# Kernel tuning notes

Measured on AMD Instinct MI355X. Metric: run time of the kernel, lower is better.

## Reference

```python
import jax, jax.numpy as jnp
import numpy as np

N, DIN, DOUT, E, K = 65536, 256, 256, 8, 2

def setup_inputs() -> dict:
    key = jax.random.key(0)
    k1, k2, k3, k4 = jax.random.split(key, 4)
    x = jax.random.normal(k1, (N, DIN), dtype=jnp.float32)
    Wr = jax.random.normal(k2, (DIN, E), dtype=jnp.float32) * (DIN ** -0.5)   # router Linear (no bias)
    We = jax.random.normal(k3, (E, DIN, DOUT), dtype=jnp.float32) * (DIN ** -0.5)  # expert Linear weights
    be = jax.random.normal(k4, (E, DOUT), dtype=jnp.float32) * 0.01               # expert Linear biases
    return {"x": x, "Wr": Wr, "We": We, "be": be}

def reference(x, Wr, We, be):
    # router: softmax over experts (eval mode -> no noise)
    probs = jax.nn.softmax(x @ Wr, axis=1)                    # [N, E]
    w, sel = jax.lax.top_k(probs, K)                          # [N, K]
    w = w / jnp.sum(w, axis=1, keepdims=True)                 # renormalize top-k weights
    # dense combine weights: scatter top-k weights back to [N, E]
    combine = jnp.zeros_like(probs).at[jnp.arange(x.shape[0])[:, None], sel].add(w)
    # all-expert outputs, then weighted combine (same math as gather/matmul/index_add loop)
    y_all = jnp.einsum('ni,eio->neo', x, We) + be[None, :, :]  # [N, E, DOUT]
    out = jnp.einsum('neo,ne->no', y_all, combine)             # [N, DOUT]
    return out
```

## Files before the change

kernel.cpp:

```cpp
#include <hip/hip_runtime.h>

#define N_TOK 65536
#define DIN   256
#define DOUT  256
#define NEXP  8
#define NPAIR 28

typedef __bf16 bf16x8 __attribute__((ext_vector_type(8)));
typedef __bf16 bf16x4 __attribute__((ext_vector_type(4)));
typedef float  f32x4  __attribute__((ext_vector_type(4)));

__device__ __forceinline__ void cp16_g2l(const void* g, void* l) {
  auto gp = (const __attribute__((address_space(1))) unsigned int*)(unsigned long long)g;
  auto lp = (__attribute__((address_space(3))) unsigned int*)(unsigned long long)l;
  __builtin_amdgcn_global_load_lds(gp, lp, 16, 0, 0);
}

__global__ __launch_bounds__(256) void prep_kernel(const float* __restrict__ We,
                                                   __bf16* __restrict__ Wt,
                                                   int* __restrict__ cnt) {
  __shared__ float T[64 * 65];
  int bid = blockIdx.x;
  if (bid == 0 && threadIdx.x < NPAIR) cnt[threadIdx.x] = 0;
  int e = bid >> 4;
  int tk = (bid >> 2) & 3, tn = bid & 3;
  int k0 = tk * 64, n0 = tn * 64;
  int tid = threadIdx.x;
  int cr = tid >> 6;
  int cc = tid & 63;
#pragma unroll
  for (int i = 0; i < 16; i++) {
    int k = i * 4 + cr;
    T[cc * 65 + k] = We[(size_t)(e * 256 + k0 + k) * 256 + n0 + cc];
  }
  __syncthreads();
#pragma unroll
  for (int i = 0; i < 16; i++) {
    int n = i * 4 + cr;
    Wt[(size_t)(e * 256 + n0 + n) * 256 + k0 + cc] = (__bf16)T[n * 65 + cc];
  }
}

__global__ __launch_bounds__(256) void router_kernel(const float* __restrict__ x,
                                                     const float* __restrict__ Wr,
                                                     __bf16* __restrict__ xb,
                                                     int* __restrict__ cnt,
                                                     unsigned short* __restrict__ pidx,
                                                     float* __restrict__ pw) {
  __shared__ float WrL[DIN * NEXP];
  __shared__ int lcnt[NPAIR];
  __shared__ int gbase[NPAIR];
  int tid = threadIdx.x;
  for (int j = tid; j < DIN * NEXP / 4; j += 256)
    *(float4*)&WrL[j * 4] = *(const float4*)&Wr[j * 4];
  if (tid < NPAIR) lcnt[tid] = 0;
  __syncthreads();

  int token = blockIdx.x * 256 + tid;
  const float4* xr = (const float4*)(x + (size_t)token * DIN);
  __bf16* xbr = xb + (size_t)token * DIN;

  float acc[NEXP];
#pragma unroll
  for (int e = 0; e < NEXP; e++) acc[e] = 0.f;

#pragma unroll 8
  for (int i4 = 0; i4 < DIN / 4; i4++) {
    float4 v = xr[i4];
    bf16x4 bv;
    bv[0] = (__bf16)v.x; bv[1] = (__bf16)v.y; bv[2] = (__bf16)v.z; bv[3] = (__bf16)v.w;
    *(bf16x4*)(xbr + i4 * 4) = bv;
    const float* w0 = &WrL[(i4 * 4) * NEXP];
#pragma unroll
    for (int e = 0; e < NEXP; e++)
      acc[e] += v.x * w0[e] + v.y * w0[NEXP + e] + v.z * w0[2 * NEXP + e] + v.w * w0[3 * NEXP + e];
  }

  int best = 0;
#pragma unroll
  for (int e = 1; e < NEXP; e++) if (acc[e] > acc[best]) best = e;
  int sec = (best == 0) ? 1 : 0;
#pragma unroll
  for (int e = 0; e < NEXP; e++)
    if (e != best && e != sec && acc[e] > acc[sec]) sec = e;
  float l3 = -1e30f;
#pragma unroll
  for (int e = 0; e < NEXP; e++)
    if (e != best && e != sec) l3 = fmaxf(l3, acc[e]);

  float diff = acc[sec] - acc[best];
  bool need = (acc[sec] - l3) < 5e-3f;
  if (__any(need)) {
    if (need) {
      double d[NEXP];
#pragma unroll
      for (int e = 0; e < NEXP; e++) d[e] = 0.0;
      for (int i4 = 0; i4 < DIN / 4; i4++) {
        float4 v = xr[i4];
        const float* w0 = &WrL[(i4 * 4) * NEXP];
#pragma unroll
        for (int e = 0; e < NEXP; e++)
          d[e] += (double)v.x * w0[e] + (double)v.y * w0[NEXP + e] +
                  (double)v.z * w0[2 * NEXP + e] + (double)v.w * w0[3 * NEXP + e];
      }
      best = 0;
#pragma unroll
      for (int e = 1; e < NEXP; e++) if (d[e] > d[best]) best = e;
      sec = (best == 0) ? 1 : 0;
#pragma unroll
      for (int e = 0; e < NEXP; e++)
        if (e != best && e != sec && d[e] > d[sec]) sec = e;
      diff = (float)(d[sec] - d[best]);
    }
  }

  float wb = 1.f / (1.f + expf(diff));
  int a, b2; float wa;
  if (best < sec) { a = best; b2 = sec; wa = wb; }
  else            { a = sec;  b2 = best; wa = 1.f - wb; }
  int p = a * (15 - a) / 2 + (b2 - a - 1);

  int lpos = atomicAdd(&lcnt[p], 1);
  __syncthreads();
  if (tid < NPAIR) gbase[tid] = atomicAdd(&cnt[tid], lcnt[tid]);
  __syncthreads();
  int pos = gbase[p] + lpos;
  pidx[p * N_TOK + pos] = (unsigned short)token;
  pw[p * N_TOK + pos] = wa;
}

__global__ __launch_bounds__(256) void moe_gemm_kernel(const __bf16* __restrict__ xb,
                                                       const __bf16* __restrict__ Wt,
                                                       const float* __restrict__ be,
                                                       const int* __restrict__ cnt,
                                                       const unsigned short* __restrict__ pidx,
                                                       const float* __restrict__ pw,
                                                       float* __restrict__ out) {
  __shared__ __bf16 As[128 * 64];
  __shared__ unsigned short tokL[128];
  __shared__ float wL[128];
  __shared__ int meta[4];

  int tid = threadIdx.x;
  int tile = blockIdx.x >> 2;
  int nh = blockIdx.x & 3;

  if (tid == 0) {
    int s = 0, pp = -1, lt = 0, c = 0;
    for (int q = 0; q < NPAIR; q++) {
      int cq = cnt[q];
      int tq = (cq + 127) >> 7;
      if (tile < s + tq) { pp = q; lt = tile - s; c = cq; break; }
      s += tq;
    }
    meta[0] = pp; meta[1] = lt; meta[2] = c;
  }
  __syncthreads();
  int p = meta[0];
  if (p < 0) return;
  int lt = meta[1], cnt_p = meta[2];

  int a = 0, rem = p;
  while (rem >= 7 - a) { rem -= 7 - a; a++; }
  int b2 = a + 1 + rem;
  int r0 = lt * 128;

  if (tid < 128) {
    int gr = r0 + tid;
    tokL[tid] = (gr < cnt_p) ? pidx[p * N_TOK + gr] : (unsigned short)0;
    wL[tid]   = (gr < cnt_p) ? pw[p * N_TOK + gr] : 0.f;
  }
  __syncthreads();

  const int lane = tid & 63, wid = tid >> 6;
  const int wm = wid & 1, wn = wid >> 1;
  const int c16 = lane & 15, quad = lane >> 4;

  const int r_base = tid >> 3;
  const int s8 = (tid & 7) ^ (r_base & 7);
  size_t grow[4];
#pragma unroll
  for (int i = 0; i < 4; i++)
    grow[i] = (size_t)tokL[r_base + 32 * i] * DIN + s8 * 8;

  const __bf16* WtA = Wt + ((size_t)a * DOUT + nh * 64) * DIN;
  const __bf16* WtB = Wt + ((size_t)b2 * DOUT + nh * 64) * DIN;

  f32x4 accA[4][2], accB[4][2];
#pragma unroll
  for (int mi = 0; mi < 4; mi++)
#pragma unroll
    for (int ni = 0; ni < 2; ni++)
#pragma unroll
      for (int r = 0; r < 4; r++) { accA[mi][ni][r] = 0.f; accB[mi][ni][r] = 0.f; }

  for (int kc = 0; kc < 4; kc++) {
#pragma unroll
    for (int i = 0; i < 4; i++) {
      int slot = tid + 256 * i;
      cp16_g2l(xb + grow[i] + kc * 64, &As[slot * 8]);
    }
    __builtin_amdgcn_s_waitcnt(0x0F70);
    __syncthreads();
#pragma unroll
    for (int ks = 0; ks < 2; ks++) {
      bf16x8 af[4], ba[2], bb[2];
#pragma unroll
      for (int mi = 0; mi < 4; mi++) {
        int row = wm * 64 + mi * 16 + c16;
        int oct = ks * 4 + quad;
        af[mi] = *(const bf16x8*)&As[(row * 8 + (oct ^ (row & 7))) * 8];
      }
#pragma unroll
      for (int ni = 0; ni < 2; ni++) {
        int col = wn * 32 + ni * 16 + c16;
        int koff = kc * 64 + ks * 32 + quad * 8;
        ba[ni] = *(const bf16x8*)&WtA[(size_t)col * DIN + koff];
        bb[ni] = *(const bf16x8*)&WtB[(size_t)col * DIN + koff];
      }
#pragma unroll
      for (int mi = 0; mi < 4; mi++)
#pragma unroll
        for (int ni = 0; ni < 2; ni++) {
          accA[mi][ni] = __builtin_amdgcn_mfma_f32_16x16x32_bf16(af[mi], ba[ni], accA[mi][ni], 0, 0, 0);
          accB[mi][ni] = __builtin_amdgcn_mfma_f32_16x16x32_bf16(af[mi], bb[ni], accB[mi][ni], 0, 0, 0);
        }
    }
    __syncthreads();
  }

#pragma unroll
  for (int ni = 0; ni < 2; ni++) {
    int gcol = nh * 64 + wn * 32 + ni * 16 + c16;
    float bea = be[a * DOUT + gcol];
    float beb = be[b2 * DOUT + gcol];
#pragma unroll
    for (int mi = 0; mi < 4; mi++) {
#pragma unroll
      for (int r = 0; r < 4; r++) {
        int row = wm * 64 + mi * 16 + quad * 4 + r;
        if (r0 + row < cnt_p) {
          float w = wL[row];
          out[(size_t)tokL[row] * DOUT + gcol] =
              w * (accA[mi][ni][r] + bea) + (1.f - w) * (accB[mi][ni][r] + beb);
        }
      }
    }
  }
}

extern "C" void kernel_launch(void* const* d_in, const int* in_sizes, int n_in,
                              void* d_out, int out_size, void* d_ws, size_t ws_size,
                              hipStream_t stream) {
  const float* x  = (const float*)d_in[0];
  const float* Wr = (const float*)d_in[1];
  const float* We = (const float*)d_in[2];
  const float* be = (const float*)d_in[3];
  float* out = (float*)d_out;

  char* w = (char*)d_ws;
  __bf16* Wt = (__bf16*)w;
  __bf16* xb = (__bf16*)(w + (1u << 20));
  int* cnt = (int*)(w + (33u << 20));
  unsigned short* pidx = (unsigned short*)(w + (33u << 20) + 512);
  float* pw = (float*)(w + (33u << 20) + 512 + (size_t)NPAIR * N_TOK * 2);

  prep_kernel<<<128, 256, 0, stream>>>(We, Wt, cnt);
  router_kernel<<<N_TOK / 256, 256, 0, stream>>>(x, Wr, xb, cnt, pidx, pw);
  moe_gemm_kernel<<<540 * 4, 256, 0, stream>>>(xb, Wt, be, cnt, pidx, pw, out);
}
```

Before: 224.1 us.

## Split router across four lanes per token and stage full A tile once in GEMM

The prep kernel now uses smaller 32x32 transpose tiles across more blocks. The router assigns four threads per token with a transposed router weight layout and reduces the partial dot products with shuffles, which gives more parallelism and coalesced loads. The grouped GEMM loads the whole 128x256 activation tile into LDS once per block and loops over all four output quarters, so the gathered rows are no longer fetched four times. The cost is 64KB of LDS per block, which limits occupancy to about two blocks per CU, and fewer GEMM blocks overall.

```diff
diff --git a/kernel.cpp b/kernel.cpp
--- a/kernel.cpp
+++ b/kernel.cpp
@@ -19,25 +19,25 @@
 __global__ __launch_bounds__(256) void prep_kernel(const float* __restrict__ We,
                                                    __bf16* __restrict__ Wt,
                                                    int* __restrict__ cnt) {
-  __shared__ float T[64 * 65];
+  __shared__ float T[32 * 33];
   int bid = blockIdx.x;
   if (bid == 0 && threadIdx.x < NPAIR) cnt[threadIdx.x] = 0;
-  int e = bid >> 4;
-  int tk = (bid >> 2) & 3, tn = bid & 3;
-  int k0 = tk * 64, n0 = tn * 64;
+  int e = bid >> 6;
+  int t = bid & 63;
+  int k0 = (t >> 3) * 32, n0 = (t & 7) * 32;
   int tid = threadIdx.x;
-  int cr = tid >> 6;
-  int cc = tid & 63;
-#pragma unroll
-  for (int i = 0; i < 16; i++) {
-    int k = i * 4 + cr;
-    T[cc * 65 + k] = We[(size_t)(e * 256 + k0 + k) * 256 + n0 + cc];
-  }
-  __syncthreads();
-#pragma unroll
-  for (int i = 0; i < 16; i++) {
-    int n = i * 4 + cr;
-    Wt[(size_t)(e * 256 + n0 + n) * 256 + k0 + cc] = (__bf16)T[n * 65 + cc];
+  int cc = tid & 31;
+  int rr = tid >> 5;
+#pragma unroll
+  for (int i = 0; i < 4; i++) {
+    int k = i * 8 + rr;
+    T[cc * 33 + k] = We[(size_t)(e * 256 + k0 + k) * 256 + n0 + cc];
+  }
+  __syncthreads();
+#pragma unroll
+  for (int i = 0; i < 4; i++) {
+    int n = i * 8 + rr;
+    Wt[(size_t)(e * 256 + n0 + n) * 256 + k0 + cc] = (__bf16)T[n * 33 + cc];
   }
 }
 
@@ -47,61 +47,74 @@
                                                      int* __restrict__ cnt,
                                                      unsigned short* __restrict__ pidx,
                                                      float* __restrict__ pw) {
-  __shared__ float WrL[DIN * NEXP];
+  __shared__ float WrT[NEXP * DIN];
   __shared__ int lcnt[NPAIR];
   __shared__ int gbase[NPAIR];
   int tid = threadIdx.x;
-  for (int j = tid; j < DIN * NEXP / 4; j += 256)
-    *(float4*)&WrL[j * 4] = *(const float4*)&Wr[j * 4];
+  for (int i = tid; i < NEXP * DIN; i += 256) {
+    int e = i >> 8, d = i & 255;
+    WrT[i] = Wr[d * NEXP + e];
+  }
   if (tid < NPAIR) lcnt[tid] = 0;
   __syncthreads();
 
-  int token = blockIdx.x * 256 + tid;
-  const float4* xr = (const float4*)(x + (size_t)token * DIN);
-  __bf16* xbr = xb + (size_t)token * DIN;
+  int token = blockIdx.x * 64 + (tid >> 2);
+  int q = tid & 3;
+  const float* xrow = x + (size_t)token * DIN;
+  const float4* xr4 = (const float4*)xrow;
+  __bf16* xbrow = xb + (size_t)token * DIN;
 
   float acc[NEXP];
 #pragma unroll
   for (int e = 0; e < NEXP; e++) acc[e] = 0.f;
 
-#pragma unroll 8
-  for (int i4 = 0; i4 < DIN / 4; i4++) {
-    float4 v = xr[i4];
+#pragma unroll 4
+  for (int j = 0; j < 16; j++) {
+    int c = j * 4 + q;
+    float4 v = xr4[c];
     bf16x4 bv;
     bv[0] = (__bf16)v.x; bv[1] = (__bf16)v.y; bv[2] = (__bf16)v.z; bv[3] = (__bf16)v.w;
-    *(bf16x4*)(xbr + i4 * 4) = bv;
-    const float* w0 = &WrL[(i4 * 4) * NEXP];
+    *(bf16x4*)(xbrow + c * 4) = bv;
+#pragma unroll
+    for (int e = 0; e < NEXP; e++) {
+      float4 w = *(const float4*)&WrT[e * DIN + c * 4];
+      acc[e] += v.x * w.x + v.y * w.y + v.z * w.z + v.w * w.w;
+    }
+  }
+#pragma unroll
+  for (int e = 0; e < NEXP; e++) {
+    acc[e] += __shfl_xor(acc[e], 1);
+    acc[e] += __shfl_xor(acc[e], 2);
+  }
+
+  int p = -1, lpos = 0, a = 0, b2 = 0;
+  float wa = 0.f;
+  if (q == 0) {
+    int best = 0;
+#pragma unroll
+    for (int e = 1; e < NEXP; e++) if (acc[e] > acc[best]) best = e;
+    int sec = (best == 0) ? 1 : 0;
 #pragma unroll
     for (int e = 0; e < NEXP; e++)
-      acc[e] += v.x * w0[e] + v.y * w0[NEXP + e] + v.z * w0[2 * NEXP + e] + v.w * w0[3 * NEXP + e];
-  }
-
-  int best = 0;
-#pragma unroll
-  for (int e = 1; e < NEXP; e++) if (acc[e] > acc[best]) best = e;
-  int sec = (best == 0) ? 1 : 0;
-#pragma unroll
-  for (int e = 0; e < NEXP; e++)
-    if (e != best && e != sec && acc[e] > acc[sec]) sec = e;
-  float l3 = -1e30f;
-#pragma unroll
-  for (int e = 0; e < NEXP; e++)
-    if (e != best && e != sec) l3 = fmaxf(l3, acc[e]);
-
-  float diff = acc[sec] - acc[best];
-  bool need = (acc[sec] - l3) < 5e-3f;
-  if (__any(need)) {
-    if (need) {
+      if (e != best && e != sec && acc[e] > acc[sec]) sec = e;
+    float l3 = -1e30f;
+#pragma unroll
+    for (int e = 0; e < NEXP; e++)
+      if (e != best && e != sec) l3 = fmaxf(l3, acc[e]);
+
+    float diff = acc[sec] - acc[best];
+    if (acc[sec] - l3 < 5e-3f) {
       double d[NEXP];
 #pragma unroll
       for (int e = 0; e < NEXP; e++) d[e] = 0.0;
-      for (int i4 = 0; i4 < DIN / 4; i4++) {
-        float4 v = xr[i4];
-        const float* w0 = &WrL[(i4 * 4) * NEXP];
-#pragma unroll
-        for (int e = 0; e < NEXP; e++)
-          d[e] += (double)v.x * w0[e] + (double)v.y * w0[NEXP + e] +
-                  (double)v.z * w0[2 * NEXP + e] + (double)v.w * w0[3 * NEXP + e];
+      for (int c = 0; c < 64; c++) {
+        float4 v = xr4[c];
+#pragma unroll
+        for (int e = 0; e < NEXP; e++) {
+          const float* w = &WrT[e * DIN + c * 4];
+          d[e] += (double)v.x * w[0] + (double)v.y * w[1] +
+                  (double)v.z * w[2] + (double)v.w * w[3];
+        }
       }
       best = 0;
 #pragma unroll
@@ -112,45 +125,47 @@
         if (e != best && e != sec && d[e] > d[sec]) sec = e;
       diff = (float)(d[sec] - d[best]);
     }
-  }
-
-  float wb = 1.f / (1.f + expf(diff));
-  int a, b2; float wa;
-  if (best < sec) { a = best; b2 = sec; wa = wb; }
-  else            { a = sec;  b2 = best; wa = 1.f - wb; }
-  int p = a * (15 - a) / 2 + (b2 - a - 1);
-
-  int lpos = atomicAdd(&lcnt[p], 1);
+
+    float wb = 1.f / (1.f + expf(diff));
+    if (best < sec) { a = best; b2 = sec; wa = wb; }
+    else            { a = sec;  b2 = best; wa = 1.f - wb; }
+    p = a * (15 - a) / 2 + (b2 - a - 1);
+    lpos = atomicAdd(&lcnt[p], 1);
+  }
   __syncthreads();
   if (tid < NPAIR) gbase[tid] = atomicAdd(&cnt[tid], lcnt[tid]);
   __syncthreads();
-  int pos = gbase[p] + lpos;
-  pidx[p * N_TOK + pos] = (unsigned short)token;
-  pw[p * N_TOK + pos] = wa;
-}
-
-__global__ __launch_bounds__(256) void moe_gemm_kernel(const __bf16* __restrict__ xb,
-                                                       const __bf16* __restrict__ Wt,
-                                                       const float* __restrict__ be,
-                                                       const int* __restrict__ cnt,
-                                                       const unsigned short* __restrict__ pidx,
-                                                       const float* __restrict__ pw,
-                                                       float* __restrict__ out) {
-  __shared__ __bf16 As[128 * 64];
+  if (q == 0) {
+    int pos = gbase[p] + lpos;
+    pidx[p * N_TOK + pos] = (unsigned short)token;
+    pw[p * N_TOK + pos] = wa;
+  }
+}
+
+__global__ __launch_bounds__(256, 2) void moe_gemm_kernel(const __bf16* __restrict__ xb,
+                                                          const __bf16* __restrict__ Wt,
+                                                          const float* __restrict__ be,
+                                                          const int* __restrict__ cnt,
+                                                          const unsigned short* __restrict__ pidx,
+                                                          const float* __restrict__ pw,
+                                                          float* __restrict__ out) {
+  __shared__ __bf16 As[128 * 256];
   __shared__ unsigned short tokL[128];
   __shared__ float wL[128];
-  __shared__ int meta[4];
+  __shared__ int cntL[NPAIR];
+  __shared__ int meta[3];
 
   int tid = threadIdx.x;
-  int tile = blockIdx.x >> 2;
-  int nh = blockIdx.x & 3;
-
+  int tile = blockIdx.x;
+
+  if (tid < NPAIR) cntL[tid] = cnt[tid];
+  __syncthreads();
   if (tid == 0) {
     int s = 0, pp = -1, lt = 0, c = 0;
-    for (int q = 0; q < NPAIR; q++) {
-      int cq = cnt[q];
+    for (int qq = 0; qq < NPAIR; qq++) {
+      int cq = cntL[qq];
       int tq = (cq + 127) >> 7;
-      if (tile < s + tq) { pp = q; lt = tile - s; c = cq; break; }
+      if (tile < s + tq) { pp = qq; lt = tile - s; c = cq; break; }
       s += tq;
     }
     meta[0] = pp; meta[1] = lt; meta[2] = c;
@@ -172,49 +187,45 @@
   }
   __syncthreads();
 
+#pragma unroll
+  for (int i = 0; i < 16; i++) {
+    int g = tid + 256 * i;
+    int r = g >> 5, sl = g & 31;
+    int s = sl ^ (r & 7);
+    cp16_g2l(xb + (size_t)tokL[r] * DIN + s * 8, &As[g * 8]);
+  }
+  __builtin_amdgcn_s_waitcnt(0x0F70);
+  __syncthreads();
+
   const int lane = tid & 63, wid = tid >> 6;
   const int wm = wid & 1, wn = wid >> 1;
   const int c16 = lane & 15, quad = lane >> 4;
 
-  const int r_base = tid >> 3;
-  const int s8 = (tid & 7) ^ (r_base & 7);
-  size_t grow[4];
-#pragma unroll
-  for (int i = 0; i < 4; i++)
-    grow[i] = (size_t)tokL[r_base + 32 * i] * DIN + s8 * 8;
-
-  const __bf16* WtA = Wt + ((size_t)a * DOUT + nh * 64) * DIN;
-  const __bf16* WtB = Wt + ((size_t)b2 * DOUT + nh * 64) * DIN;
-
-  f32x4 accA[4][2], accB[4][2];
-#pragma unroll
-  for (int mi = 0; mi < 4; mi++)
-#pragma unroll
-    for (int ni = 0; ni < 2; ni++)
-#pragma unroll
-      for (int r = 0; r < 4; r++) { accA[mi][ni][r] = 0.f; accB[mi][ni][r] = 0.f; }
-
-  for (int kc = 0; kc < 4; kc++) {
-#pragma unroll
-    for (int i = 0; i < 4; i++) {
-      int slot = tid + 256 * i;
-      cp16_g2l(xb + grow[i] + kc * 64, &As[slot * 8]);
-    }
-    __builtin_amdgcn_s_waitcnt(0x0F70);
-    __syncthreads();
-#pragma unroll
-    for (int ks = 0; ks < 2; ks++) {
+  const __bf16* WtA = Wt + (size_t)a  * DOUT * DIN;
+  const __bf16* WtB = Wt + (size_t)b2 * DOUT * DIN;
+
+  for (int nh = 0; nh < 4; nh++) {
+    f32x4 accA[4][2], accB[4][2];
+#pragma unroll
+    for (int mi = 0; mi < 4; mi++)
+#pragma unroll
+      for (int ni = 0; ni < 2; ni++)
+#pragma unroll
+        for (int r = 0; r < 4; r++) { accA[mi][ni][r] = 0.f; accB[mi][ni][r] = 0.f; }
+
+#pragma unroll
+    for (int kstep = 0; kstep < 8; kstep++) {
       bf16x8 af[4], ba[2], bb[2];
+      int o = kstep * 4 + quad;
 #pragma unroll
       for (int mi = 0; mi < 4; mi++) {
         int row = wm * 64 + mi * 16 + c16;
-        int oct = ks * 4 + quad;
-        af[mi] = *(const bf16x8*)&As[(row * 8 + (oct ^ (row & 7))) * 8];
-      }
+        af[mi] = *(const bf16x8*)&As[row * 256 + (o ^ (row & 7)) * 8];
+      }
+      int koff = kstep * 32 + quad * 8;
 #pragma unroll
       for (int ni = 0; ni < 2; ni++) {
-        int col = wn * 32 + ni * 16 + c16;
-        int koff = kc * 64 + ks * 32 + quad * 8;
+        int col = nh * 64 + wn * 32 + ni * 16 + c16;
         ba[ni] = *(const bf16x8*)&WtA[(size_t)col * DIN + koff];
         bb[ni] = *(const bf16x8*)&WtB[(size_t)col * DIN + koff];
       }
@@ -226,23 +237,22 @@
           accB[mi][ni] = __builtin_amdgcn_mfma_f32_16x16x32_bf16(af[mi], bb[ni], accB[mi][ni], 0, 0, 0);
         }
     }
-    __syncthreads();
-  }
-
-#pragma unroll
-  for (int ni = 0; ni < 2; ni++) {
-    int gcol = nh * 64 + wn * 32 + ni * 16 + c16;
-    float bea = be[a * DOUT + gcol];
-    float beb = be[b2 * DOUT + gcol];
-#pragma unroll
-    for (int mi = 0; mi < 4; mi++) {
-#pragma unroll
-      for (int r = 0; r < 4; r++) {
-        int row = wm * 64 + mi * 16 + quad * 4 + r;
-        if (r0 + row < cnt_p) {
-          float w = wL[row];
-          out[(size_t)tokL[row] * DOUT + gcol] =
-              w * (accA[mi][ni][r] + bea) + (1.f - w) * (accB[mi][ni][r] + beb);
+
+#pragma unroll
+    for (int ni = 0; ni < 2; ni++) {
+      int gcol = nh * 64 + wn * 32 + ni * 16 + c16;
+      float bea = be[a * DOUT + gcol];
+      float beb = be[b2 * DOUT + gcol];
+#pragma unroll
+      for (int mi = 0; mi < 4; mi++) {
+#pragma unroll
+        for (int r = 0; r < 4; r++) {
+          int row = wm * 64 + mi * 16 + quad * 4 + r;
+          if (r0 + row < cnt_p) {
+            float w = wL[row];
+            out[(size_t)tokL[row] * DOUT + gcol] =
+                w * (accA[mi][ni][r] + bea) + (1.f - w) * (accB[mi][ni][r] + beb);
+          }
         }
       }
     }
@@ -265,7 +275,7 @@
   unsigned short* pidx = (unsigned short*)(w + (33u << 20) + 512);
   float* pw = (float*)(w + (33u << 20) + 512 + (size_t)NPAIR * N_TOK * 2);
 
-  prep_kernel<<<128, 256, 0, stream>>>(We, Wt, cnt);
-  router_kernel<<<N_TOK / 256, 256, 0, stream>>>(x, Wr, xb, cnt, pidx, pw);
-  moe_gemm_kernel<<<540 * 4, 256, 0, stream>>>(xb, Wt, be, cnt, pidx, pw, out);
-}
+  prep_kernel<<<512, 256, 0, stream>>>(We, Wt, cnt);
+  router_kernel<<<N_TOK / 64, 256, 0, stream>>>(x, Wr, xb, cnt, pidx, pw);
+  moe_gemm_kernel<<<540, 256, 0, stream>>>(xb, Wt, be, cnt, pidx, pw, out);
+}
```

Result: slower. 295.3 us (+31.7%).
